# Kernel optimization log

Measured on AMD Instinct MI355X. Metric: run time of the kernel, lower is better.

## Reference

```python
import jax, jax.numpy as jnp
import numpy as np
import math

B, C, D, H, W = 8, 128, 64, 32, 32
SHRINK = C // 2  # 64
EPS = 1e-5


def setup_inputs() -> dict:
    key = jax.random.key(0)
    ks = jax.random.split(key, 7)
    x = jax.random.normal(ks[0], (B, C, D, H, W), dtype=jnp.float32)
    # 1x1x1 Conv3d weights collapse to [out_ch, in_ch] matrices (no bias)
    def kaiming(k, shape):
        fan_in = shape[1]
        return jax.random.normal(k, shape, dtype=jnp.float32) * np.float32(math.sqrt(2.0 / fan_in))
    Wk = kaiming(ks[1], (SHRINK, C))
    Wq = kaiming(ks[2], (SHRINK, C))
    Wv = kaiming(ks[3], (SHRINK, C))
    Wo = kaiming(ks[4], (C, SHRINK))
    gamma = jnp.ones((C,), dtype=jnp.float32)
    beta = jnp.zeros((C,), dtype=jnp.float32)
    return {"x": x, "Wk": Wk, "Wq": Wq, "Wv": Wv, "Wo": Wo, "gamma": gamma, "beta": beta}


def reference(x, Wk, Wq, Wv, Wo, gamma, beta):
    b, c, d, h, w = x.shape
    s = Wk.shape[0]
    # BatchNorm3d (training mode: batch statistics over B, D, H, W)
    mean = jnp.mean(x, axis=(0, 2, 3, 4), keepdims=True)
    var = jnp.var(x, axis=(0, 2, 3, 4), keepdims=True)
    xn = (x - mean) * jax.lax.rsqrt(var + EPS)
    xn = xn * gamma[None, :, None, None, None] + beta[None, :, None, None, None]
    # fold spatial into batch: [B*H*W, C, D]
    xr = jnp.transpose(xn, (0, 3, 4, 1, 2)).reshape(b * h * w, c, d)
    k = jnp.einsum('sc,ncd->nsd', Wk, xr)  # [N, S, D]
    q = jnp.einsum('sc,ncd->nsd', Wq, xr)
    v = jnp.einsum('sc,ncd->nsd', Wv, xr)
    scores = jnp.einsum('nsi,nsj->nij', k, q) / jnp.float32(math.sqrt(s))  # [N, D, D]
    a = jax.nn.softmax(scores, axis=1)  # softmax over key-time axis (dim=1)
    attn = jnp.einsum('nsi,nij->nsj', v, a)  # [N, S, D]
    attn = attn.reshape(b, h, w, s, d)
    out = jnp.einsum('os,bhwsd->bodhw', Wo, attn)  # 1x1x1 conv out proj
    return x + out
```

## Files before the change

### kernel.cpp

```cpp
#include <hip/hip_runtime.h>

typedef __attribute__((ext_vector_type(8))) short short8;
typedef __attribute__((ext_vector_type(4))) float f32x4;
typedef unsigned short u16;
typedef unsigned int u32;

#define CNT_PER_C (8*64*32*32)

#define WS_PART  0
#define WS_SCALE 8192
#define WS_SHIFT 8704
#define WS_WKQV  9216
#define WS_WO    58368
#define WS_OUTP  131072

__device__ __forceinline__ u16 f2bf(float f){
  u32 u = __builtin_bit_cast(u32, f);
  u32 r = u + 0x7FFFu + ((u >> 16) & 1u);
  return (u16)(r >> 16);
}
__device__ __forceinline__ float bf2f(u16 h){
  u32 u = ((u32)h) << 16;
  return __builtin_bit_cast(float, u);
}
__device__ __forceinline__ u32 pk2(float a, float b){
  return (u32)f2bf(a) | ((u32)f2bf(b) << 16);
}

__global__ void k_prep(const float* wk, const float* wq, const float* wv,
                       const float* wo, u16* wkqv_bf, u16* wo_bf){
  int idx = blockIdx.x*1024 + threadIdx.x*4;
#pragma unroll
  for (int i=0;i<4;i++){
    int id = idx+i;
    if (id < 24576){
      int r = id >> 7, c = id & 127;
      float v = (r<64) ? wk[r*128+c] : (r<128) ? wq[(r-64)*128+c] : wv[(r-128)*128+c];
      wkqv_bf[id] = f2bf(v);
    } else {
      int j = id - 24576;
      wo_bf[j] = f2bf(wo[j]);
    }
  }
}

__global__ __launch_bounds__(256) void k_stats1(const float* x, float* part){
  int cb = blockIdx.x; int c = cb>>3, b = cb&7;
  const float4* p = (const float4*)(x + ((size_t)(b*128 + c))*65536);
  int t = threadIdx.x;
  float s=0.f, s2=0.f;
  for (int i=0;i<64;i++){
    float4 v = p[t + i*256];
    s  += v.x+v.y+v.z+v.w;
    s2 += v.x*v.x + v.y*v.y + v.z*v.z + v.w*v.w;
  }
  for (int off=32; off; off>>=1){ s += __shfl_down(s, off, 64); s2 += __shfl_down(s2, off, 64); }
  __shared__ float ls[8];
  int wid = t>>6, lane = t&63;
  if (lane==0){ ls[wid*2]=s; ls[wid*2+1]=s2; }
  __syncthreads();
  if (t==0){
    float S=0.f, S2=0.f;
    for (int wv=0; wv<4; wv++){ S+=ls[wv*2]; S2+=ls[wv*2+1]; }
    part[cb*2]=S; part[cb*2+1]=S2;
  }
}

__global__ void k_stats2(const float* part, const float* gamma, const float* beta,
                         float* scale, float* shift){
  int c = threadIdx.x;
  float S=0.f, S2=0.f;
  for (int b=0;b<8;b++){ S += part[(c*8+b)*2]; S2 += part[(c*8+b)*2+1]; }
  float inv = 1.0f/(float)CNT_PER_C;
  float mean = S*inv;
  float var  = S2*inv - mean*mean;
  float rstd = rsqrtf(var + 1e-5f);
  float sc = gamma[c]*rstd;
  scale[c] = sc; shift[c] = beta[c] - mean*sc;
}

__global__ __launch_bounds__(256) void k_norm_t(const float* x, const float* scale,
                                                const float* shift, u16* xn_t){
  __shared__ u16 lm[32*512];
  __shared__ float lsc[128], lsh[128];
  int t = threadIdx.x;
  if (t < 128){ lsc[t] = scale[t]; lsh[t] = shift[t]; }
  int bid = blockIdx.x;
  int bh = bid>>3, dq = bid&7;
  int b = bh>>5, h = bh&31;
  int d0 = dq*8, n0 = bh*32;
  int s = t>>3, q = t&7;
  __syncthreads();
  for (int h2=0; h2<2; h2++){
    int w4 = q*4;
#pragma unroll
    for (int i=0;i<16;i++){
      int rowpos = i*32 + s;
      int cl = rowpos & 63, dd = rowpos >> 6;
      int c = h2*64 + cl;
      float4 v = *(const float4*)(x + ((size_t)((b*128 + c)*64 + d0 + dd))*1024 + h*32 + w4);
      float sc = lsc[c], sh = lsh[c];
      lm[(w4+0)*512 + (rowpos ^ ((w4+0)&28))] = f2bf(v.x*sc + sh);
      lm[(w4+1)*512 + (rowpos ^ ((w4+1)&28))] = f2bf(v.y*sc + sh);
      lm[(w4+2)*512 + (rowpos ^ ((w4+2)&28))] = f2bf(v.z*sc + sh);
      lm[(w4+3)*512 + (rowpos ^ ((w4+3)&28))] = f2bf(v.w*sc + sh);
    }
    __syncthreads();
    {
      int n = s, oct = q;
      int oq = oct ^ ((n>>3)&3);
      bool swp = (n & 4) != 0;
#pragma unroll
      for (int m=0;m<8;m++){
        uint4 raw = *(const uint4*)&lm[n*512 + m*64 + oq*8];
        if (swp){ u32 tx=raw.x, ty=raw.y; raw.x=raw.z; raw.y=raw.w; raw.z=tx; raw.w=ty; }
        *(uint4*)(xn_t + (size_t)(n0+n)*8192 + (size_t)(d0+m)*128 + h2*64 + oct*8) = raw;
      }
    }
    __syncthreads();
  }
}

__global__ __launch_bounds__(256, 2) void k_attn(const u16* __restrict__ xn_t,
                                                 const u16* __restrict__ wkqv,
                                                 const u16* __restrict__ wo,
                                                 u16* __restrict__ out_pre){
  __shared__ alignas(16) char smb[65536];
  const int t = threadIdx.x, lane = t & 63, wid = t >> 6;
  const int lr = lane & 15, lk = lane >> 4;
  const int n = blockIdx.x*4 + wid;
  char* slot = smb + wid*16384;
  char* lo = slot;
  char* hi = slot + 8192;
  const u16* xg = xn_t + (size_t)n*8192;

  short8 xbf[4][4];
#pragma unroll
  for (int ct=0; ct<4; ct++)
#pragma unroll
    for (int ks=0; ks<4; ks++)
      xbf[ct][ks] = *(const short8*)(xg + (ct*16+lr)*128 + ks*32 + lk*8);

#pragma unroll
  for (int mt=0; mt<4; mt++){
    short8 af[4];
#pragma unroll
    for (int ks=0; ks<4; ks++)
      af[ks] = *(const short8*)(wkqv + (size_t)(mt*16 + lr)*128 + ks*32 + lk*8);
#pragma unroll
    for (int ct=0; ct<4; ct++){
      f32x4 a = (f32x4){0.f,0.f,0.f,0.f};
#pragma unroll
      for (int ks=0; ks<4; ks++)
        a = __builtin_amdgcn_mfma_f32_16x16x32_bf16(af[ks], xbf[ct][ks], a, 0,0,0);
      int d = ct*16 + lr;
      *(uint2*)(lo + d*128 + ((mt*32 + lk*8) ^ ((d&7)<<4))) =
        (uint2){pk2(a[0],a[1]), pk2(a[2],a[3])};
    }
  }
#pragma unroll
  for (int mt=0; mt<4; mt++){
    short8 af[4];
#pragma unroll
    for (int ks=0; ks<4; ks++)
      af[ks] = *(const short8*)(wkqv + (size_t)((mt+4)*16 + lr)*128 + ks*32 + lk*8);
#pragma unroll
    for (int ct=0; ct<4; ct++){
      f32x4 a = (f32x4){0.f,0.f,0.f,0.f};
#pragma unroll
      for (int ks=0; ks<4; ks++)
        a = __builtin_amdgcn_mfma_f32_16x16x32_bf16(af[ks], xbf[ct][ks], a, 0,0,0);
      int d = ct*16 + lr;
      *(uint2*)(hi + d*128 + ((mt*32 + lk*8) ^ ((d&7)<<4))) =
        (uint2){pk2(a[0],a[1]), pk2(a[2],a[3])};
    }
  }
  f32x4 vacc[4][4];
#pragma unroll
  for (int mt=0; mt<4; mt++){
    short8 af[4];
#pragma unroll
    for (int ks=0; ks<4; ks++)
      af[ks] = *(const short8*)(wkqv + (size_t)((mt+8)*16 + lr)*128 + ks*32 + lk*8);
#pragma unroll
    for (int ct=0; ct<4; ct++) vacc[mt][ct] = (f32x4){0.f,0.f,0.f,0.f};
#pragma unroll
    for (int ct=0; ct<4; ct++)
#pragma unroll
      for (int ks=0; ks<4; ks++)
        vacc[mt][ct] = __builtin_amdgcn_mfma_f32_16x16x32_bf16(af[ks], xbf[ct][ks], vacc[mt][ct], 0,0,0);
  }

  short8 ka[4][2];
#pragma unroll
  for (int it=0; it<4; it++)
#pragma unroll
    for (int ks2=0; ks2<2; ks2++){
      int i = it*16 + lr;
      ka[it][ks2] = *(const short8*)(lo + i*128 + ((ks2*64 + lk*16) ^ ((i&7)<<4)));
    }
#pragma unroll
  for (int m4=0; m4<4; m4++)
#pragma unroll
    for (int ct=0; ct<4; ct++)
#pragma unroll
      for (int e=0; e<4; e++){
        int sp = m4*16 + lk*4 + e, i = ct*16 + lr;
        *(u16*)(lo + sp*128 + ((i*2) ^ ((sp&7)<<4))) = f2bf(vacc[m4][ct][e]);
      }
  short8 qb[4][2];
#pragma unroll
  for (int jt=0; jt<4; jt++)
#pragma unroll
    for (int ks2=0; ks2<2; ks2++){
      int j = jt*16 + lr;
      qb[jt][ks2] = *(const short8*)(hi + j*128 + ((ks2*64 + lk*16) ^ ((j&7)<<4)));
    }
  f32x4 sc4[4][4];
#pragma unroll
  for (int it=0; it<4; it++)
#pragma unroll
    for (int jt=0; jt<4; jt++) sc4[it][jt] = (f32x4){0.f,0.f,0.f,0.f};
#pragma unroll
  for (int it=0; it<4; it++)
#pragma unroll
    for (int jt=0; jt<4; jt++)
#pragma unroll
      for (int ks2=0; ks2<2; ks2++)
        sc4[it][jt] = __builtin_amdgcn_mfma_f32_16x16x32_bf16(ka[it][ks2], qb[jt][ks2], sc4[it][jt], 0,0,0);

#pragma unroll
  for (int jt=0; jt<4; jt++){
    float m = -1e30f;
#pragma unroll
    for (int it=0; it<4; it++)
#pragma unroll
      for (int e=0; e<4; e++) m = fmaxf(m, sc4[it][jt][e]);
    m = fmaxf(m, __shfl_xor(m, 16, 64));
    m = fmaxf(m, __shfl_xor(m, 32, 64));
    float ssum = 0.f;
#pragma unroll
    for (int it=0; it<4; it++)
#pragma unroll
      for (int e=0; e<4; e++){
        float p = __expf((sc4[it][jt][e] - m) * 0.125f);
        sc4[it][jt][e] = p; ssum += p;
      }
    ssum += __shfl_xor(ssum, 16, 64);
    ssum += __shfl_xor(ssum, 32, 64);
    float inv = 1.0f / ssum;
    int j = jt*16 + lr;
#pragma unroll
    for (int it=0; it<4; it++){
      *(uint2*)(hi + j*128 + ((it*32 + lk*8) ^ ((j&7)<<4))) =
        (uint2){pk2(sc4[it][jt][0]*inv, sc4[it][jt][1]*inv),
                pk2(sc4[it][jt][2]*inv, sc4[it][jt][3]*inv)};
    }
  }

  short8 va[4][2], ab[4][2];
#pragma unroll
  for (int st=0; st<4; st++)
#pragma unroll
    for (int ks2=0; ks2<2; ks2++){
      int s2 = st*16 + lr;
      va[st][ks2] = *(const short8*)(lo + s2*128 + ((ks2*64 + lk*16) ^ ((s2&7)<<4)));
    }
#pragma unroll
  for (int jt=0; jt<4; jt++)
#pragma unroll
    for (int ks2=0; ks2<2; ks2++){
      int j = jt*16 + lr;
      ab[jt][ks2] = *(const short8*)(hi + j*128 + ((ks2*64 + lk*16) ^ ((j&7)<<4)));
    }
  f32x4 at4[4][4];
#pragma unroll
  for (int st=0; st<4; st++)
#pragma unroll
    for (int jt=0; jt<4; jt++) at4[st][jt] = (f32x4){0.f,0.f,0.f,0.f};
#pragma unroll
  for (int st=0; st<4; st++)
#pragma unroll
    for (int jt=0; jt<4; jt++)
#pragma unroll
      for (int ks2=0; ks2<2; ks2++)
        at4[st][jt] = __builtin_amdgcn_mfma_f32_16x16x32_bf16(va[st][ks2], ab[jt][ks2], at4[st][jt], 0,0,0);
#pragma unroll
  for (int st=0; st<4; st++)
#pragma unroll
    for (int jt=0; jt<4; jt++){
      int d = jt*16 + lr;
      *(uint2*)(lo + d*128 + ((st*32 + lk*8) ^ ((d&7)<<4))) =
        (uint2){pk2(at4[st][jt][0], at4[st][jt][1]), pk2(at4[st][jt][2], at4[st][jt][3])};
    }

  short8 tb[4][2];
#pragma unroll
  for (int dt=0; dt<4; dt++)
#pragma unroll
    for (int ks2=0; ks2<2; ks2++){
      int d = dt*16 + lr;
      tb[dt][ks2] = *(const short8*)(lo + d*128 + ((ks2*64 + lk*16) ^ ((d&7)<<4)));
    }
#pragma unroll
  for (int mt=0; mt<8; mt++){
    short8 wa[2];
#pragma unroll
    for (int ks2=0; ks2<2; ks2++)
      wa[ks2] = *(const short8*)(wo + (size_t)(mt*16 + lr)*64 + ks2*32 + lk*8);
    f32x4 oa[4];
#pragma unroll
    for (int dt=0; dt<4; dt++) oa[dt] = (f32x4){0.f,0.f,0.f,0.f};
#pragma unroll
    for (int dt=0; dt<4; dt++)
#pragma unroll
      for (int ks2=0; ks2<2; ks2++)
        oa[dt] = __builtin_amdgcn_mfma_f32_16x16x32_bf16(wa[ks2], tb[dt][ks2], oa[dt], 0,0,0);
#pragma unroll
    for (int dt=0; dt<4; dt++)
#pragma unroll
      for (int e=0; e<4; e++){
        int cc = mt*16 + lk*4 + e, d = dt*16 + lr;
        *(u16*)(slot + cc*128 + ((d*2) ^ ((cc&7)<<4))) = f2bf(oa[dt][e]);
      }
  }

  u16* og = out_pre + (size_t)n*8192;
#pragma unroll
  for (int r=0;r<16;r++){
    int j = r*64 + lane;
    int cc = j>>3, o = j&7;
    uint4 v = *(const uint4*)(slot + cc*128 + ((o*16) ^ ((cc&7)<<4)));
    *(uint4*)(og + j*8) = v;
  }
}

__global__ __launch_bounds__(256) void k_merge(const float* x, const u16* out_pre, float* out){
  __shared__ u16 lm[32*512];
  int t = threadIdx.x;
  int bid = blockIdx.x;
  int bh = bid>>2, cq = bid&3;
  int b = bh>>5, h = bh&31;
  int n0 = bh*32;
  int cbase = cq*32;
  int s = t>>3, q = t&7;
  for (int cc=0; cc<4; cc++){
    int cb = cbase + cc*8;
    {
      int n = s;
      int oq = q ^ ((n>>3)&3);
      bool swp = (n & 4) != 0;
#pragma unroll
      for (int i=0;i<8;i++){
        uint4 raw = *(const uint4*)(out_pre + (size_t)(n0+n)*8192 + (cb+i)*64 + q*8);
        if (swp){ u32 tx=raw.x, ty=raw.y; raw.x=raw.z; raw.y=raw.w; raw.z=tx; raw.w=ty; }
        *(uint4*)&lm[n*512 + i*64 + oq*8] = raw;
      }
    }
    __syncthreads();
    {
      int w4 = q*4;
#pragma unroll
      for (int g=0; g<16; g++){
        int row = g*32 + s;
        int ci = row>>6, d = row&63;
        size_t gi = ((size_t)((b*128 + cb + ci)*64 + d))*1024 + h*32 + w4;
        float4 xv = *(const float4*)(x + gi);
        float4 ov;
        ov.x = xv.x + bf2f(lm[(w4+0)*512 + (row ^ ((w4+0)&28))]);
        ov.y = xv.y + bf2f(lm[(w4+1)*512 + (row ^ ((w4+1)&28))]);
        ov.z = xv.z + bf2f(lm[(w4+2)*512 + (row ^ ((w4+2)&28))]);
        ov.w = xv.w + bf2f(lm[(w4+3)*512 + (row ^ ((w4+3)&28))]);
        *(float4*)(out + gi) = ov;
      }
    }
    __syncthreads();
  }
}

extern "C" void kernel_launch(void* const* d_in, const int* in_sizes, int n_in,
                              void* d_out, int out_size, void* d_ws, size_t ws_size,
                              hipStream_t stream){
  const float* x     = (const float*)d_in[0];
  const float* Wk    = (const float*)d_in[1];
  const float* Wq    = (const float*)d_in[2];
  const float* Wv    = (const float*)d_in[3];
  const float* Wo    = (const float*)d_in[4];
  const float* gamma = (const float*)d_in[5];
  const float* beta  = (const float*)d_in[6];
  float* out = (float*)d_out;
  char* ws = (char*)d_ws;

  float* part  = (float*)(ws + WS_PART);
  float* scale = (float*)(ws + WS_SCALE);
  float* shift = (float*)(ws + WS_SHIFT);
  u16* wkqv  = (u16*)(ws + WS_WKQV);
  u16* wo_bf = (u16*)(ws + WS_WO);
  u16* outp  = (u16*)(ws + WS_OUTP);
  u16* xn_t  = (u16*)d_out;

  k_prep  <<<32,   256, 0, stream>>>(Wk, Wq, Wv, Wo, wkqv, wo_bf);
  k_stats1<<<1024, 256, 0, stream>>>(x, part);
  k_stats2<<<1,    128, 0, stream>>>(part, gamma, beta, scale, shift);
  k_norm_t<<<2048, 256, 0, stream>>>(x, scale, shift, xn_t);
  k_attn  <<<2048, 256, 0, stream>>>(xn_t, wkqv, wo_bf, outp);
  k_merge <<<1024, 256, 0, stream>>>(x, outp, out);
}
```

Measured before the change: 387.7 us.

## Halve per-wave LDS in attention kernel to double occupancy

Each wave's LDS scratch shrinks from 16 KB to 8 KB by reusing a single buffer. K and Q fragments are read back right after each is written, probabilities are normalized in registers before the buffer is reused, and the output projection is staged and written out in two halves. Launch bounds go from 2 to 4 blocks per CU to exploit the freed shared memory. The cost is more register pressure, since ka and qb now stay live across the V projection, which may cause spills or cap the achieved occupancy.

```diff
diff --git a/kernel.cpp b/kernel.cpp
--- a/kernel.cpp
+++ b/kernel.cpp
@@ -121,17 +121,15 @@
   }
 }
 
-__global__ __launch_bounds__(256, 2) void k_attn(const u16* __restrict__ xn_t,
+__global__ __launch_bounds__(256, 4) void k_attn(const u16* __restrict__ xn_t,
                                                  const u16* __restrict__ wkqv,
                                                  const u16* __restrict__ wo,
                                                  u16* __restrict__ out_pre){
-  __shared__ alignas(16) char smb[65536];
+  __shared__ alignas(16) char smb[32768];
   const int t = threadIdx.x, lane = t & 63, wid = t >> 6;
   const int lr = lane & 15, lk = lane >> 4;
   const int n = blockIdx.x*4 + wid;
-  char* slot = smb + wid*16384;
-  char* lo = slot;
-  char* hi = slot + 8192;
+  char* slot = smb + wid*8192;
   const u16* xg = xn_t + (size_t)n*8192;
 
   short8 xbf[4][4];
@@ -154,10 +152,19 @@
       for (int ks=0; ks<4; ks++)
         a = __builtin_amdgcn_mfma_f32_16x16x32_bf16(af[ks], xbf[ct][ks], a, 0,0,0);
       int d = ct*16 + lr;
-      *(uint2*)(lo + d*128 + ((mt*32 + lk*8) ^ ((d&7)<<4))) =
+      *(uint2*)(slot + d*128 + ((mt*32 + lk*8) ^ ((d&7)<<4))) =
         (uint2){pk2(a[0],a[1]), pk2(a[2],a[3])};
     }
   }
+  short8 ka[4][2];
+#pragma unroll
+  for (int it=0; it<4; it++)
+#pragma unroll
+    for (int ks2=0; ks2<2; ks2++){
+      int i = it*16 + lr;
+      ka[it][ks2] = *(const short8*)(slot + i*128 + ((ks2*64 + lk*16) ^ ((i&7)<<4)));
+    }
+
 #pragma unroll
   for (int mt=0; mt<4; mt++){
     short8 af[4];
@@ -171,10 +178,19 @@
       for (int ks=0; ks<4; ks++)
         a = __builtin_amdgcn_mfma_f32_16x16x32_bf16(af[ks], xbf[ct][ks], a, 0,0,0);
       int d = ct*16 + lr;
-      *(uint2*)(hi + d*128 + ((mt*32 + lk*8) ^ ((d&7)<<4))) =
+      *(uint2*)(slot + d*128 + ((mt*32 + lk*8) ^ ((d&7)<<4))) =
         (uint2){pk2(a[0],a[1]), pk2(a[2],a[3])};
     }
   }
+  short8 qb[4][2];
+#pragma unroll
+  for (int jt=0; jt<4; jt++)
+#pragma unroll
+    for (int ks2=0; ks2<2; ks2++){
+      int j = jt*16 + lr;
+      qb[jt][ks2] = *(const short8*)(slot + j*128 + ((ks2*64 + lk*16) ^ ((j&7)<<4)));
+    }
+
   f32x4 vacc[4][4];
 #pragma unroll
   for (int mt=0; mt<4; mt++){
@@ -190,15 +206,6 @@
       for (int ks=0; ks<4; ks++)
         vacc[mt][ct] = __builtin_amdgcn_mfma_f32_16x16x32_bf16(af[ks], xbf[ct][ks], vacc[mt][ct], 0,0,0);
   }
-
-  short8 ka[4][2];
-#pragma unroll
-  for (int it=0; it<4; it++)
-#pragma unroll
-    for (int ks2=0; ks2<2; ks2++){
-      int i = it*16 + lr;
-      ka[it][ks2] = *(const short8*)(lo + i*128 + ((ks2*64 + lk*16) ^ ((i&7)<<4)));
-    }
 #pragma unroll
   for (int m4=0; m4<4; m4++)
 #pragma unroll
@@ -206,16 +213,9 @@
 #pragma unroll
       for (int e=0; e<4; e++){
         int sp = m4*16 + lk*4 + e, i = ct*16 + lr;
-        *(u16*)(lo + sp*128 + ((i*2) ^ ((sp&7)<<4))) = f2bf(vacc[m4][ct][e]);
+        *(u16*)(slot + sp*128 + ((i*2) ^ ((sp&7)<<4))) = f2bf(vacc[m4][ct][e]);
       }
-  short8 qb[4][2];
-#pragma unroll
-  for (int jt=0; jt<4; jt++)
-#pragma unroll
-    for (int ks2=0; ks2<2; ks2++){
-      int j = jt*16 + lr;
-      qb[jt][ks2] = *(const short8*)(hi + j*128 + ((ks2*64 + lk*16) ^ ((j&7)<<4)));
-    }
+
   f32x4 sc4[4][4];
 #pragma unroll
   for (int it=0; it<4; it++)
@@ -249,30 +249,39 @@
     ssum += __shfl_xor(ssum, 16, 64);
     ssum += __shfl_xor(ssum, 32, 64);
     float inv = 1.0f / ssum;
-    int j = jt*16 + lr;
-#pragma unroll
-    for (int it=0; it<4; it++){
-      *(uint2*)(hi + j*128 + ((it*32 + lk*8) ^ ((j&7)<<4))) =
-        (uint2){pk2(sc4[it][jt][0]*inv, sc4[it][jt][1]*inv),
-                pk2(sc4[it][jt][2]*inv, sc4[it][jt][3]*inv)};
-    }
-  }
-
-  short8 va[4][2], ab[4][2];
+#pragma unroll
+    for (int it=0; it<4; it++)
+#pragma unroll
+      for (int e=0; e<4; e++) sc4[it][jt][e] *= inv;
+  }
+
+  short8 va[4][2];
 #pragma unroll
   for (int st=0; st<4; st++)
 #pragma unroll
     for (int ks2=0; ks2<2; ks2++){
       int s2 = st*16 + lr;
-      va[st][ks2] = *(const short8*)(lo + s2*128 + ((ks2*64 + lk*16) ^ ((s2&7)<<4)));
-    }
+      va[st][ks2] = *(const short8*)(slot + s2*128 + ((ks2*64 + lk*16) ^ ((s2&7)<<4)));
+    }
+#pragma unroll
+  for (int jt=0; jt<4; jt++){
+    int j = jt*16 + lr;
+#pragma unroll
+    for (int it=0; it<4; it++){
+      *(uint2*)(slot + j*128 + ((it*32 + lk*8) ^ ((j&7)<<4))) =
+        (uint2){pk2(sc4[it][jt][0], sc4[it][jt][1]),
+                pk2(sc4[it][jt][2], sc4[it][jt][3])};
+    }
+  }
+  short8 ab[4][2];
 #pragma unroll
   for (int jt=0; jt<4; jt++)
 #pragma unroll
     for (int ks2=0; ks2<2; ks2++){
       int j = jt*16 + lr;
-      ab[jt][ks2] = *(const short8*)(hi + j*128 + ((ks2*64 + lk*16) ^ ((j&7)<<4)));
-    }
+      ab[jt][ks2] = *(const short8*)(slot + j*128 + ((ks2*64 + lk*16) ^ ((j&7)<<4)));
+    }
+
   f32x4 at4[4][4];
 #pragma unroll
   for (int st=0; st<4; st++)
@@ -290,48 +299,50 @@
 #pragma unroll
     for (int jt=0; jt<4; jt++){
       int d = jt*16 + lr;
-      *(uint2*)(lo + d*128 + ((st*32 + lk*8) ^ ((d&7)<<4))) =
+      *(uint2*)(slot + d*128 + ((st*32 + lk*8) ^ ((d&7)<<4))) =
         (uint2){pk2(at4[st][jt][0], at4[st][jt][1]), pk2(at4[st][jt][2], at4[st][jt][3])};
     }
-
   short8 tb[4][2];
 #pragma unroll
   for (int dt=0; dt<4; dt++)
 #pragma unroll
     for (int ks2=0; ks2<2; ks2++){
       int d = dt*16 + lr;
-      tb[dt][ks2] = *(const short8*)(lo + d*128 + ((ks2*64 + lk*16) ^ ((d&7)<<4)));
-    }
-#pragma unroll
-  for (int mt=0; mt<8; mt++){
-    short8 wa[2];
-#pragma unroll
-    for (int ks2=0; ks2<2; ks2++)
-      wa[ks2] = *(const short8*)(wo + (size_t)(mt*16 + lr)*64 + ks2*32 + lk*8);
-    f32x4 oa[4];
-#pragma unroll
-    for (int dt=0; dt<4; dt++) oa[dt] = (f32x4){0.f,0.f,0.f,0.f};
-#pragma unroll
-    for (int dt=0; dt<4; dt++)
+      tb[dt][ks2] = *(const short8*)(slot + d*128 + ((ks2*64 + lk*16) ^ ((d&7)<<4)));
+    }
+
+  u16* og = out_pre + (size_t)n*8192;
+#pragma unroll
+  for (int hf=0; hf<2; hf++){
+#pragma unroll
+    for (int mt=0; mt<4; mt++){
+      short8 wa[2];
 #pragma unroll
       for (int ks2=0; ks2<2; ks2++)
-        oa[dt] = __builtin_amdgcn_mfma_f32_16x16x32_bf16(wa[ks2], tb[dt][ks2], oa[dt], 0,0,0);
-#pragma unroll
-    for (int dt=0; dt<4; dt++)
-#pragma unroll
-      for (int e=0; e<4; e++){
-        int cc = mt*16 + lk*4 + e, d = dt*16 + lr;
-        *(u16*)(slot + cc*128 + ((d*2) ^ ((cc&7)<<4))) = f2bf(oa[dt][e]);
-      }
-  }
-
-  u16* og = out_pre + (size_t)n*8192;
-#pragma unroll
-  for (int r=0;r<16;r++){
-    int j = r*64 + lane;
-    int cc = j>>3, o = j&7;
-    uint4 v = *(const uint4*)(slot + cc*128 + ((o*16) ^ ((cc&7)<<4)));
-    *(uint4*)(og + j*8) = v;
+        wa[ks2] = *(const short8*)(wo + (size_t)((hf*4+mt)*16 + lr)*64 + ks2*32 + lk*8);
+      f32x4 oa[4];
+#pragma unroll
+      for (int dt=0; dt<4; dt++) oa[dt] = (f32x4){0.f,0.f,0.f,0.f};
+#pragma unroll
+      for (int dt=0; dt<4; dt++)
+#pragma unroll
+        for (int ks2=0; ks2<2; ks2++)
+          oa[dt] = __builtin_amdgcn_mfma_f32_16x16x32_bf16(wa[ks2], tb[dt][ks2], oa[dt], 0,0,0);
+#pragma unroll
+      for (int dt=0; dt<4; dt++)
+#pragma unroll
+        for (int e=0; e<4; e++){
+          int cl = mt*16 + lk*4 + e, d = dt*16 + lr;
+          *(u16*)(slot + cl*128 + ((d*2) ^ ((cl&7)<<4))) = f2bf(oa[dt][e]);
+        }
+    }
+#pragma unroll
+    for (int r=0;r<8;r++){
+      int j = r*64 + lane;
+      int cc = j>>3, o = j&7;
+      uint4 v = *(const uint4*)(slot + cc*128 + ((o*16) ^ ((cc&7)<<4)));
+      *(uint4*)(og + hf*4096 + j*8) = v;
+    }
   }
 }
 
```

Result: slower. 459.3 us (+18.5%).

## Reconstruct residual from normalized bf16 input instead of rereading fp32 x

Applied to the files above, without the earlier changes.

The residual add moves into the attention kernel, where x is rebuilt from the bf16 normalized tensor by inverting the BatchNorm affine (xn/scale - shift/scale). The merge kernel then no longer reads the 128MB fp32 input, saving a full-size HBM read. The cost is that the residual now carries bf16 quantisation error and is stored in bf16 out_pre. It also divides by gamma*rstd, which is unstable if gamma is near zero.

```diff
diff --git a/kernel.cpp b/kernel.cpp
--- a/kernel.cpp
+++ b/kernel.cpp
@@ -12,6 +12,8 @@
 #define WS_SHIFT 8704
 #define WS_WKQV  9216
 #define WS_WO    58368
+#define WS_RS    74752
+#define WS_RB    75264
 #define WS_OUTP  131072
 
 __device__ __forceinline__ u16 f2bf(float f){
@@ -67,7 +69,7 @@
 }
 
 __global__ void k_stats2(const float* part, const float* gamma, const float* beta,
-                         float* scale, float* shift){
+                         float* scale, float* shift, float* rs, float* rb){
   int c = threadIdx.x;
   float S=0.f, S2=0.f;
   for (int b=0;b<8;b++){ S += part[(c*8+b)*2]; S2 += part[(c*8+b)*2+1]; }
@@ -76,7 +78,10 @@
   float var  = S2*inv - mean*mean;
   float rstd = rsqrtf(var + 1e-5f);
   float sc = gamma[c]*rstd;
-  scale[c] = sc; shift[c] = beta[c] - mean*sc;
+  float sh = beta[c] - mean*sc;
+  scale[c] = sc; shift[c] = sh;
+  rs[c] = 1.0f/sc;
+  rb[c] = -sh/sc;
 }
 
 __global__ __launch_bounds__(256) void k_norm_t(const float* x, const float* scale,
@@ -124,6 +129,8 @@
 __global__ __launch_bounds__(256, 2) void k_attn(const u16* __restrict__ xn_t,
                                                  const u16* __restrict__ wkqv,
                                                  const u16* __restrict__ wo,
+                                                 const float* __restrict__ rs,
+                                                 const float* __restrict__ rb,
                                                  u16* __restrict__ out_pre){
   __shared__ alignas(16) char smb[65536];
   const int t = threadIdx.x, lane = t & 63, wid = t >> 6;
@@ -316,6 +323,16 @@
 #pragma unroll
       for (int ks2=0; ks2<2; ks2++)
         oa[dt] = __builtin_amdgcn_mfma_f32_16x16x32_bf16(wa[ks2], tb[dt][ks2], oa[dt], 0,0,0);
+    float4 rs4 = *(const float4*)(rs + mt*16 + lk*4);
+    float4 rb4 = *(const float4*)(rb + mt*16 + lk*4);
+#pragma unroll
+    for (int dt=0; dt<4; dt++){
+      ushort4 xv = *(const ushort4*)(xg + (size_t)(dt*16+lr)*128 + mt*16 + lk*4);
+      oa[dt][0] += bf2f(xv.x)*rs4.x + rb4.x;
+      oa[dt][1] += bf2f(xv.y)*rs4.y + rb4.y;
+      oa[dt][2] += bf2f(xv.z)*rs4.z + rb4.z;
+      oa[dt][3] += bf2f(xv.w)*rs4.w + rb4.w;
+    }
 #pragma unroll
     for (int dt=0; dt<4; dt++)
 #pragma unroll
@@ -335,7 +352,7 @@
   }
 }
 
-__global__ __launch_bounds__(256) void k_merge(const float* x, const u16* out_pre, float* out){
+__global__ __launch_bounds__(256) void k_merge(const u16* out_pre, float* out){
   __shared__ u16 lm[32*512];
   int t = threadIdx.x;
   int bid = blockIdx.x;
@@ -365,12 +382,11 @@
         int row = g*32 + s;
         int ci = row>>6, d = row&63;
         size_t gi = ((size_t)((b*128 + cb + ci)*64 + d))*1024 + h*32 + w4;
-        float4 xv = *(const float4*)(x + gi);
         float4 ov;
-        ov.x = xv.x + bf2f(lm[(w4+0)*512 + (row ^ ((w4+0)&28))]);
-        ov.y = xv.y + bf2f(lm[(w4+1)*512 + (row ^ ((w4+1)&28))]);
-        ov.z = xv.z + bf2f(lm[(w4+2)*512 + (row ^ ((w4+2)&28))]);
-        ov.w = xv.w + bf2f(lm[(w4+3)*512 + (row ^ ((w4+3)&28))]);
+        ov.x = bf2f(lm[(w4+0)*512 + (row ^ ((w4+0)&28))]);
+        ov.y = bf2f(lm[(w4+1)*512 + (row ^ ((w4+1)&28))]);
+        ov.z = bf2f(lm[(w4+2)*512 + (row ^ ((w4+2)&28))]);
+        ov.w = bf2f(lm[(w4+3)*512 + (row ^ ((w4+3)&28))]);
         *(float4*)(out + gi) = ov;
       }
     }
@@ -394,6 +410,8 @@
   float* part  = (float*)(ws + WS_PART);
   float* scale = (float*)(ws + WS_SCALE);
   float* shift = (float*)(ws + WS_SHIFT);
+  float* rsp   = (float*)(ws + WS_RS);
+  float* rbp   = (float*)(ws + WS_RB);
   u16* wkqv  = (u16*)(ws + WS_WKQV);
   u16* wo_bf = (u16*)(ws + WS_WO);
   u16* outp  = (u16*)(ws + WS_OUTP);
@@ -401,8 +419,8 @@
 
   k_prep  <<<32,   256, 0, stream>>>(Wk, Wq, Wv, Wo, wkqv, wo_bf);
   k_stats1<<<1024, 256, 0, stream>>>(x, part);
-  k_stats2<<<1,    128, 0, stream>>>(part, gamma, beta, scale, shift);
+  k_stats2<<<1,    128, 0, stream>>>(part, gamma, beta, scale, shift, rsp, rbp);
   k_norm_t<<<2048, 256, 0, stream>>>(x, scale, shift, xn_t);
-  k_attn  <<<2048, 256, 0, stream>>>(xn_t, wkqv, wo_bf, outp);
-  k_merge <<<1024, 256, 0, stream>>>(x, outp, out);
-}
+  k_attn  <<<2048, 256, 0, stream>>>(xn_t, wkqv, wo_bf, rsp, rbp, outp);
+  k_merge <<<1024, 256, 0, stream>>>(outp, out);
+}
```

New measurement: 361.3 us. 6.8% less time.

## Fold BatchNorm into projection weights and fuse stats with transpose

Applied to the files above, without the earlier changes.

BatchNorm scale is folded into the K/Q/V projection weights and the shift into a per-row bias. That lets the kernel compute channel statistics in the same pass that transposes raw x to bf16, instead of running a separate statistics pass over x. The residual is now added inside the attention kernel from the bf16 transposed x, so the merge kernel no longer rereads fp32 x. Together this removes roughly two full fp32 reads of x. The cost is that the residual now carries bf16 precision, and the statistics step adds atomics and a small single-block weight-prep kernel.

```diff
diff --git a/kernel.cpp b/kernel.cpp
--- a/kernel.cpp
+++ b/kernel.cpp
@@ -10,8 +10,9 @@
 #define WS_PART  0
 #define WS_SCALE 8192
 #define WS_SHIFT 8704
-#define WS_WKQV  9216
-#define WS_WO    58368
+#define WS_BIAS  9216
+#define WS_WKQV  10240
+#define WS_WO    59392
 #define WS_OUTP  131072
 
 __device__ __forceinline__ u16 f2bf(float f){
@@ -27,50 +28,69 @@
   return (u32)f2bf(a) | ((u32)f2bf(b) << 16);
 }
 
-__global__ void k_prep(const float* wk, const float* wq, const float* wv,
-                       const float* wo, u16* wkqv_bf, u16* wo_bf){
-  int idx = blockIdx.x*1024 + threadIdx.x*4;
-#pragma unroll
-  for (int i=0;i<4;i++){
-    int id = idx+i;
-    if (id < 24576){
-      int r = id >> 7, c = id & 127;
-      float v = (r<64) ? wk[r*128+c] : (r<128) ? wq[(r-64)*128+c] : wv[(r-128)*128+c];
-      wkqv_bf[id] = f2bf(v);
-    } else {
-      int j = id - 24576;
-      wo_bf[j] = f2bf(wo[j]);
-    }
-  }
-}
-
-__global__ __launch_bounds__(256) void k_stats1(const float* x, float* part){
-  int cb = blockIdx.x; int c = cb>>3, b = cb&7;
-  const float4* p = (const float4*)(x + ((size_t)(b*128 + c))*65536);
+__global__ void k_zero(float* part){
+  part[blockIdx.x*256 + threadIdx.x] = 0.f;
+}
+
+__global__ __launch_bounds__(256) void k_stats_t(const float* __restrict__ x,
+                                                 u16* __restrict__ x_t,
+                                                 float* __restrict__ part){
+  __shared__ u16 lm[32*512];
+  __shared__ float cs[256];
   int t = threadIdx.x;
-  float s=0.f, s2=0.f;
-  for (int i=0;i<64;i++){
-    float4 v = p[t + i*256];
-    s  += v.x+v.y+v.z+v.w;
-    s2 += v.x*v.x + v.y*v.y + v.z*v.z + v.w*v.w;
-  }
-  for (int off=32; off; off>>=1){ s += __shfl_down(s, off, 64); s2 += __shfl_down(s2, off, 64); }
-  __shared__ float ls[8];
-  int wid = t>>6, lane = t&63;
-  if (lane==0){ ls[wid*2]=s; ls[wid*2+1]=s2; }
+  cs[t] = 0.f;
+  int bid = blockIdx.x;
+  int bh = bid>>3, dq = bid&7;
+  int b = bh>>5, h = bh&31;
+  int d0 = dq*8, n0 = bh*32;
+  int s = t>>3, q = t&7;
+  float sA=0.f,qA=0.f, sB=0.f,qB=0.f, sC=0.f,qC=0.f, sD=0.f,qD=0.f;
   __syncthreads();
-  if (t==0){
-    float S=0.f, S2=0.f;
-    for (int wv=0; wv<4; wv++){ S+=ls[wv*2]; S2+=ls[wv*2+1]; }
-    part[cb*2]=S; part[cb*2+1]=S2;
-  }
+#pragma unroll
+  for (int h2=0; h2<2; h2++){
+    int w4 = q*4;
+#pragma unroll
+    for (int i=0;i<16;i++){
+      int rowpos = i*32 + s;
+      int cl = rowpos & 63, dd = rowpos >> 6;
+      int c = h2*64 + cl;
+      float4 v = *(const float4*)(x + ((size_t)((b*128 + c)*64 + d0 + dd))*1024 + h*32 + w4);
+      float lsum = v.x+v.y+v.z+v.w;
+      float lsq  = v.x*v.x+v.y*v.y+v.z*v.z+v.w*v.w;
+      if (h2==0){ if ((i&1)==0){ sA+=lsum; qA+=lsq; } else { sB+=lsum; qB+=lsq; } }
+      else      { if ((i&1)==0){ sC+=lsum; qC+=lsq; } else { sD+=lsum; qD+=lsq; } }
+      lm[(w4+0)*512 + (rowpos ^ ((w4+0)&28))] = f2bf(v.x);
+      lm[(w4+1)*512 + (rowpos ^ ((w4+1)&28))] = f2bf(v.y);
+      lm[(w4+2)*512 + (rowpos ^ ((w4+2)&28))] = f2bf(v.z);
+      lm[(w4+3)*512 + (rowpos ^ ((w4+3)&28))] = f2bf(v.w);
+    }
+    __syncthreads();
+    {
+      int n = s, oct = q;
+      int oq = oct ^ ((n>>3)&3);
+      bool swp = (n & 4) != 0;
+#pragma unroll
+      for (int m=0;m<8;m++){
+        uint4 raw = *(const uint4*)&lm[n*512 + m*64 + oq*8];
+        if (swp){ u32 tx=raw.x, ty=raw.y; raw.x=raw.z; raw.y=raw.w; raw.z=tx; raw.w=ty; }
+        *(uint4*)(x_t + (size_t)(n0+n)*8192 + (size_t)(d0+m)*128 + h2*64 + oct*8) = raw;
+      }
+    }
+    __syncthreads();
+  }
+  atomicAdd(&cs[(s    )*2+0], sA); atomicAdd(&cs[(s    )*2+1], qA);
+  atomicAdd(&cs[(s+32 )*2+0], sB); atomicAdd(&cs[(s+32 )*2+1], qB);
+  atomicAdd(&cs[(s+64 )*2+0], sC); atomicAdd(&cs[(s+64 )*2+1], qC);
+  atomicAdd(&cs[(s+96 )*2+0], sD); atomicAdd(&cs[(s+96 )*2+1], qD);
+  __syncthreads();
+  atomicAdd(&part[(bid&7)*256 + t], cs[t]);
 }
 
 __global__ void k_stats2(const float* part, const float* gamma, const float* beta,
                          float* scale, float* shift){
   int c = threadIdx.x;
   float S=0.f, S2=0.f;
-  for (int b=0;b<8;b++){ S += part[(c*8+b)*2]; S2 += part[(c*8+b)*2+1]; }
+  for (int i=0;i<8;i++){ S += part[i*256 + c*2]; S2 += part[i*256 + c*2 + 1]; }
   float inv = 1.0f/(float)CNT_PER_C;
   float mean = S*inv;
   float var  = S2*inv - mean*mean;
@@ -79,51 +99,28 @@
   scale[c] = sc; shift[c] = beta[c] - mean*sc;
 }
 
-__global__ __launch_bounds__(256) void k_norm_t(const float* x, const float* scale,
-                                                const float* shift, u16* xn_t){
-  __shared__ u16 lm[32*512];
-  __shared__ float lsc[128], lsh[128];
+__global__ __launch_bounds__(256) void k_wprep(const float* wk, const float* wq, const float* wv,
+                                               const float* wo, const float* scale,
+                                               const float* shift, u16* wkqv_bf, u16* wo_bf,
+                                               float* bias){
   int t = threadIdx.x;
-  if (t < 128){ lsc[t] = scale[t]; lsh[t] = shift[t]; }
-  int bid = blockIdx.x;
-  int bh = bid>>3, dq = bid&7;
-  int b = bh>>5, h = bh&31;
-  int d0 = dq*8, n0 = bh*32;
-  int s = t>>3, q = t&7;
-  __syncthreads();
-  for (int h2=0; h2<2; h2++){
-    int w4 = q*4;
-#pragma unroll
-    for (int i=0;i<16;i++){
-      int rowpos = i*32 + s;
-      int cl = rowpos & 63, dd = rowpos >> 6;
-      int c = h2*64 + cl;
-      float4 v = *(const float4*)(x + ((size_t)((b*128 + c)*64 + d0 + dd))*1024 + h*32 + w4);
-      float sc = lsc[c], sh = lsh[c];
-      lm[(w4+0)*512 + (rowpos ^ ((w4+0)&28))] = f2bf(v.x*sc + sh);
-      lm[(w4+1)*512 + (rowpos ^ ((w4+1)&28))] = f2bf(v.y*sc + sh);
-      lm[(w4+2)*512 + (rowpos ^ ((w4+2)&28))] = f2bf(v.z*sc + sh);
-      lm[(w4+3)*512 + (rowpos ^ ((w4+3)&28))] = f2bf(v.w*sc + sh);
-    }
-    __syncthreads();
-    {
-      int n = s, oct = q;
-      int oq = oct ^ ((n>>3)&3);
-      bool swp = (n & 4) != 0;
-#pragma unroll
-      for (int m=0;m<8;m++){
-        uint4 raw = *(const uint4*)&lm[n*512 + m*64 + oq*8];
-        if (swp){ u32 tx=raw.x, ty=raw.y; raw.x=raw.z; raw.y=raw.w; raw.z=tx; raw.w=ty; }
-        *(uint4*)(xn_t + (size_t)(n0+n)*8192 + (size_t)(d0+m)*128 + h2*64 + oct*8) = raw;
-      }
-    }
-    __syncthreads();
-  }
-}
-
-__global__ __launch_bounds__(256, 2) void k_attn(const u16* __restrict__ xn_t,
+  if (t < 192){
+    const float* src = (t<64) ? (wk + t*128) : (t<128) ? (wq + (t-64)*128) : (wv + (t-128)*128);
+    float bsum = 0.f;
+    for (int c=0;c<128;c++){
+      float w = src[c];
+      bsum += w*shift[c];
+      wkqv_bf[t*128+c] = f2bf(w*scale[c]);
+    }
+    bias[t] = bsum;
+  }
+  for (int j=t; j<8192; j+=256) wo_bf[j] = f2bf(wo[j]);
+}
+
+__global__ __launch_bounds__(256, 2) void k_attn(const u16* __restrict__ x_t,
                                                  const u16* __restrict__ wkqv,
                                                  const u16* __restrict__ wo,
+                                                 const float* __restrict__ bias,
                                                  u16* __restrict__ out_pre){
   __shared__ alignas(16) char smb[65536];
   const int t = threadIdx.x, lane = t & 63, wid = t >> 6;
@@ -132,7 +129,7 @@
   char* slot = smb + wid*16384;
   char* lo = slot;
   char* hi = slot + 8192;
-  const u16* xg = xn_t + (size_t)n*8192;
+  const u16* xg = x_t + (size_t)n*8192;
 
   short8 xbf[4][4];
 #pragma unroll
@@ -147,12 +144,14 @@
 #pragma unroll
     for (int ks=0; ks<4; ks++)
       af[ks] = *(const short8*)(wkqv + (size_t)(mt*16 + lr)*128 + ks*32 + lk*8);
+    float4 bk4 = *(const float4*)(bias + mt*16 + lk*4);
 #pragma unroll
     for (int ct=0; ct<4; ct++){
       f32x4 a = (f32x4){0.f,0.f,0.f,0.f};
 #pragma unroll
       for (int ks=0; ks<4; ks++)
         a = __builtin_amdgcn_mfma_f32_16x16x32_bf16(af[ks], xbf[ct][ks], a, 0,0,0);
+      a[0]+=bk4.x; a[1]+=bk4.y; a[2]+=bk4.z; a[3]+=bk4.w;
       int d = ct*16 + lr;
       *(uint2*)(lo + d*128 + ((mt*32 + lk*8) ^ ((d&7)<<4))) =
         (uint2){pk2(a[0],a[1]), pk2(a[2],a[3])};
@@ -164,12 +163,14 @@
 #pragma unroll
     for (int ks=0; ks<4; ks++)
       af[ks] = *(const short8*)(wkqv + (size_t)((mt+4)*16 + lr)*128 + ks*32 + lk*8);
+    float4 bq4 = *(const float4*)(bias + 64 + mt*16 + lk*4);
 #pragma unroll
     for (int ct=0; ct<4; ct++){
       f32x4 a = (f32x4){0.f,0.f,0.f,0.f};
 #pragma unroll
       for (int ks=0; ks<4; ks++)
         a = __builtin_amdgcn_mfma_f32_16x16x32_bf16(af[ks], xbf[ct][ks], a, 0,0,0);
+      a[0]+=bq4.x; a[1]+=bq4.y; a[2]+=bq4.z; a[3]+=bq4.w;
       int d = ct*16 + lr;
       *(uint2*)(hi + d*128 + ((mt*32 + lk*8) ^ ((d&7)<<4))) =
         (uint2){pk2(a[0],a[1]), pk2(a[2],a[3])};
@@ -182,13 +183,17 @@
 #pragma unroll
     for (int ks=0; ks<4; ks++)
       af[ks] = *(const short8*)(wkqv + (size_t)((mt+8)*16 + lr)*128 + ks*32 + lk*8);
+    float4 bv4 = *(const float4*)(bias + 128 + mt*16 + lk*4);
 #pragma unroll
     for (int ct=0; ct<4; ct++) vacc[mt][ct] = (f32x4){0.f,0.f,0.f,0.f};
 #pragma unroll
-    for (int ct=0; ct<4; ct++)
+    for (int ct=0; ct<4; ct++){
 #pragma unroll
       for (int ks=0; ks<4; ks++)
         vacc[mt][ct] = __builtin_amdgcn_mfma_f32_16x16x32_bf16(af[ks], xbf[ct][ks], vacc[mt][ct], 0,0,0);
+      vacc[mt][ct][0]+=bv4.x; vacc[mt][ct][1]+=bv4.y;
+      vacc[mt][ct][2]+=bv4.z; vacc[mt][ct][3]+=bv4.w;
+    }
   }
 
   short8 ka[4][2];
@@ -316,6 +321,14 @@
 #pragma unroll
       for (int ks2=0; ks2<2; ks2++)
         oa[dt] = __builtin_amdgcn_mfma_f32_16x16x32_bf16(wa[ks2], tb[dt][ks2], oa[dt], 0,0,0);
+#pragma unroll
+    for (int dt=0; dt<4; dt++){
+      ushort4 xv = *(const ushort4*)(xg + (size_t)(dt*16+lr)*128 + mt*16 + lk*4);
+      oa[dt][0] += bf2f(xv.x);
+      oa[dt][1] += bf2f(xv.y);
+      oa[dt][2] += bf2f(xv.z);
+      oa[dt][3] += bf2f(xv.w);
+    }
 #pragma unroll
     for (int dt=0; dt<4; dt++)
 #pragma unroll
@@ -335,7 +348,7 @@
   }
 }
 
-__global__ __launch_bounds__(256) void k_merge(const float* x, const u16* out_pre, float* out){
+__global__ __launch_bounds__(256) void k_merge(const u16* out_pre, float* out){
   __shared__ u16 lm[32*512];
   int t = threadIdx.x;
   int bid = blockIdx.x;
@@ -365,12 +378,11 @@
         int row = g*32 + s;
         int ci = row>>6, d = row&63;
         size_t gi = ((size_t)((b*128 + cb + ci)*64 + d))*1024 + h*32 + w4;
-        float4 xv = *(const float4*)(x + gi);
         float4 ov;
-        ov.x = xv.x + bf2f(lm[(w4+0)*512 + (row ^ ((w4+0)&28))]);
-        ov.y = xv.y + bf2f(lm[(w4+1)*512 + (row ^ ((w4+1)&28))]);
-        ov.z = xv.z + bf2f(lm[(w4+2)*512 + (row ^ ((w4+2)&28))]);
-        ov.w = xv.w + bf2f(lm[(w4+3)*512 + (row ^ ((w4+3)&28))]);
+        ov.x = bf2f(lm[(w4+0)*512 + (row ^ ((w4+0)&28))]);
+        ov.y = bf2f(lm[(w4+1)*512 + (row ^ ((w4+1)&28))]);
+        ov.z = bf2f(lm[(w4+2)*512 + (row ^ ((w4+2)&28))]);
+        ov.w = bf2f(lm[(w4+3)*512 + (row ^ ((w4+3)&28))]);
         *(float4*)(out + gi) = ov;
       }
     }
@@ -394,15 +406,16 @@
   float* part  = (float*)(ws + WS_PART);
   float* scale = (float*)(ws + WS_SCALE);
   float* shift = (float*)(ws + WS_SHIFT);
+  float* bias  = (float*)(ws + WS_BIAS);
   u16* wkqv  = (u16*)(ws + WS_WKQV);
   u16* wo_bf = (u16*)(ws + WS_WO);
   u16* outp  = (u16*)(ws + WS_OUTP);
-  u16* xn_t  = (u16*)d_out;
-
-  k_prep  <<<32,   256, 0, stream>>>(Wk, Wq, Wv, Wo, wkqv, wo_bf);
-  k_stats1<<<1024, 256, 0, stream>>>(x, part);
-  k_stats2<<<1,    128, 0, stream>>>(part, gamma, beta, scale, shift);
-  k_norm_t<<<2048, 256, 0, stream>>>(x, scale, shift, xn_t);
-  k_attn  <<<2048, 256, 0, stream>>>(xn_t, wkqv, wo_bf, outp);
-  k_merge <<<1024, 256, 0, stream>>>(x, outp, out);
-}
+  u16* x_t   = (u16*)d_out;
+
+  k_zero   <<<8,    256, 0, stream>>>(part);
+  k_stats_t<<<2048, 256, 0, stream>>>(x, x_t, part);
+  k_stats2 <<<1,    128, 0, stream>>>(part, gamma, beta, scale, shift);
+  k_wprep  <<<1,    256, 0, stream>>>(Wk, Wq, Wv, Wo, scale, shift, wkqv, wo_bf, bias);
+  k_attn   <<<2048, 256, 0, stream>>>(x_t, wkqv, wo_bf, bias, outp);
+  k_merge  <<<1024, 256, 0, stream>>>(outp, out);
+}
```

Result: faster. 328.0 us (-15.4%).
